# Optimization experiments

Hardware: AMD Instinct MI355X
Metric: run time of the kernel (lower is better)

The kernel has to match this reference:

```python
import jax, jax.numpy as jnp
import numpy as np

B = 64            # batch
C = 23            # chromosomes
E = 1024          # embedding_dim (eos)
D = 1024          # d_model
BOT = 128         # bottleneck_dim (embedding table width)
BINS = 8192       # bins per chromosome (num_bins_list entries)
NUM_BINS = C * BINS
S = 3             # num_states


def setup_inputs() -> dict:
    key = jax.random.key(0)
    ks = jax.random.split(key, 7)
    eos_emb = jax.random.normal(ks[0], (B, C, E), dtype=jnp.float32)
    # embedding table: indices used are 1..NUM_BINS (cum starts at 1), so NUM_BINS+2 rows
    emb_table = jax.random.normal(ks[1], (NUM_BINS + 2, BOT), dtype=jnp.float32) * 0.02
    Wb = jax.random.normal(ks[2], (D, BOT), dtype=jnp.float32) * 0.02   # bin_projection (no bias)
    We = jax.random.normal(ks[3], (D, E), dtype=jnp.float32) * 0.02     # eos_projection weight
    be = jax.random.normal(ks[4], (D,), dtype=jnp.float32) * 0.02       # eos_projection bias
    Wfc = jax.random.normal(ks[5], (S, 2 * D), dtype=jnp.float32) * 0.02  # fc weight
    bfc = jax.random.normal(ks[6], (S,), dtype=jnp.float32) * 0.02        # fc bias
    return {"eos_emb": eos_emb, "emb_table": emb_table, "Wb": Wb,
            "We": We, "be": be, "Wfc": Wfc, "bfc": bfc}


def reference(eos_emb, emb_table, Wb, We, be, Wfc, bfc):
    # eos_projection (use_eos_proj=True): [B, C, E] -> [B, C, D]
    eos = jnp.einsum('bce,de->bcd', eos_emb, We) + be
    # embedding lookup for all bins: indices 1..NUM_BINS (contiguous across chromosomes)
    idx = 1 + jnp.arange(NUM_BINS)
    # bin_projection (bottleneck_dim != d_model): [NUM_BINS, BOT] -> [NUM_BINS, D]
    bin_emb = jnp.einsum('nk,dk->nd', emb_table[idx], Wb).reshape(C, BINS, D)
    # fc on concat([bin_emb, eos]) == bin_emb @ W1^T + eos @ W2^T + b (avoids materializing concat)
    W1, W2 = Wfc[:, :D], Wfc[:, D:]
    part_bin = jnp.einsum('cnd,sd->cns', bin_emb, W1)   # [C, BINS, S]
    part_eos = jnp.einsum('bcd,sd->bcs', eos, W2)        # [B, C, S]
    # original returns list of 23 tensors [B, BINS, S]; stacked here as [B, C, BINS, S]
    out = jax.nn.relu(part_bin[None] + part_eos[:, :, None, :] + bfc)
    return out
```

## Files before the change

### kernel.cpp

```cpp
#include <hip/hip_runtime.h>

#define B_    64
#define C_    23
#define E_    1024
#define D_    1024
#define BOT_  128
#define BINS_ 8192
#define S_    3
#define NUMBINS (C_*BINS_)

typedef float f32x4 __attribute__((ext_vector_type(4)));

#define WS_M  0
#define WS_N  512
#define WS_C0 3584
#define WS_PE 3600

__global__ __launch_bounds__(256) void kprep(const float* __restrict__ Wb,
                                             const float* __restrict__ We,
                                             const float* __restrict__ be,
                                             const float* __restrict__ Wfc,
                                             const float* __restrict__ bfc,
                                             float* __restrict__ ws) {
    const int bx = blockIdx.x;
    const int t  = threadIdx.x;

    if (bx == 72) {
        int wave = t >> 6, lane = t & 63;
        if (wave < 3) {
            const float* w2 = Wfc + wave * 2 * D_ + D_;
            float acc = 0.f;
            #pragma unroll
            for (int j = 0; j < D_ / 64; j++) {
                int d = lane + j * 64;
                acc += w2[d] * be[d];
            }
            #pragma unroll
            for (int off = 32; off; off >>= 1) acc += __shfl_down(acc, off);
            if (lane == 0) ws[WS_C0 + wave] = acc + bfc[wave];
        }
        return;
    }

    __shared__ float wv[3072];
    __shared__ float red[256];

    const int og   = t & 15;
    const int dgrp = t >> 4;

    const float* src;
    int ostride, obase, wofs;
    float* dst0;
    int dstride;

    if (bx < 64) {
        int e0 = bx * 16;
        src = We; ostride = E_; obase = e0; wofs = D_;
        dst0 = ws + WS_N + e0; dstride = E_;
    } else {
        int k0 = (bx - 64) * 16;
        src = Wb; ostride = BOT_; obase = k0; wofs = 0;
        dst0 = ws + WS_M + k0; dstride = BOT_;
    }

    for (int i = t; i < 3072; i += 256) {
        int s = i >> 10, d = i & 1023;
        wv[i] = Wfc[s * 2 * D_ + wofs + d];
    }
    __syncthreads();

    const float* p  = src + (size_t)(dgrp * 64) * ostride + obase + og;
    const float* w0 = wv + dgrp * 64;
    float a0 = 0.f, a1 = 0.f, a2 = 0.f;
    #pragma unroll 8
    for (int i = 0; i < 64; i++) {
        float v = p[(size_t)i * ostride];
        a0 += w0[i] * v;
        a1 += w0[1024 + i] * v;
        a2 += w0[2048 + i] * v;
    }
    float accs[3] = {a0, a1, a2};
    for (int s = 0; s < 3; s++) {
        __syncthreads();
        red[t] = accs[s];
        #pragma unroll
        for (int off = 128; off >= 16; off >>= 1) {
            __syncthreads();
            if (t < off) red[t] += red[t + off];
        }
        if (t < 16) dst0[s * dstride + t] = red[t];
    }
}

__global__ __launch_bounds__(256) void kpe(const float* __restrict__ eos,
                                           float* ws) {
    int wave = threadIdx.x >> 6;
    int lane = threadIdx.x & 63;
    int row  = blockIdx.x * 4 + wave;
    const float* x  = eos + (size_t)row * E_;
    const float* N0 = ws + WS_N;
    float a0 = 0.f, a1 = 0.f, a2 = 0.f;
    #pragma unroll
    for (int j = 0; j < E_ / 64; j++) {
        int i = lane + j * 64;
        float v = x[i];
        a0 += v * N0[i];
        a1 += v * N0[1024 + i];
        a2 += v * N0[2048 + i];
    }
    #pragma unroll
    for (int off = 32; off; off >>= 1) {
        a0 += __shfl_down(a0, off);
        a1 += __shfl_down(a1, off);
        a2 += __shfl_down(a2, off);
    }
    if (lane == 0) {
        float* pe = ws + WS_PE + row * 3;
        pe[0] = a0 + ws[WS_C0 + 0];
        pe[1] = a1 + ws[WS_C0 + 1];
        pe[2] = a2 + ws[WS_C0 + 2];
    }
}

__global__ __launch_bounds__(256) void kmain(const float* __restrict__ table,
                                             const float* __restrict__ ws,
                                             float* __restrict__ out) {
    const int t  = threadIdx.x;
    const int c  = blockIdx.y;
    const int n0 = blockIdx.x * 256;

    const int w  = t >> 6;
    const int l  = t & 63;
    const int h  = l >> 5;
    const int kk = l & 31;

    __shared__ float P[64 * 97];
    __shared__ float pbl[768];
    __shared__ float pel[192];

    f32x4 M0 = ((const f32x4*)(ws + WS_M      ))[kk];
    f32x4 M1 = ((const f32x4*)(ws + WS_M + 128))[kk];
    f32x4 M2 = ((const f32x4*)(ws + WS_M + 256))[kk];

    if (t < 192) {
        int b = t / 3, s = t - b * 3;
        pel[t] = ws[WS_PE + (b * C_ + c) * 3 + s];
    }

    const float* base = table + (size_t)(1 + c * BINS_ + n0) * BOT_ + kk * 4;

    f32x4 va[8], vb[8];
    #pragma unroll
    for (int i = 0; i < 8; i++) {
        int rl = (w * 8 + i) * 2 + h;
        va[i] = *(const f32x4*)(base + (size_t)rl * BOT_);
    }

    #pragma unroll
    for (int bb = 0; bb < 4; bb++) {
        #pragma unroll
        for (int i = 0; i < 8; i++) {
            int rl = (w * 8 + i) * 2 + h;
            f32x4 v = (bb & 1) ? vb[i] : va[i];
            float* pp = &P[rl * 97 + kk * 3];
            pp[0] = v.x * M0.x + v.y * M0.y + v.z * M0.z + v.w * M0.w;
            pp[1] = v.x * M1.x + v.y * M1.y + v.z * M1.z + v.w * M1.w;
            pp[2] = v.x * M2.x + v.y * M2.y + v.z * M2.z + v.w * M2.w;
        }
        if (bb < 3) {
            #pragma unroll
            for (int i = 0; i < 8; i++) {
                int rl = (w * 8 + i) * 2 + h;
                f32x4 ld = *(const f32x4*)(base + (size_t)((bb + 1) * 64 + rl) * BOT_);
                if (bb & 1) va[i] = ld; else vb[i] = ld;
            }
        }
        __syncthreads();
        if (t < 192) {
            int s = t >> 6, ro = t & 63;
            const float* pr = &P[ro * 97 + s];
            float acc = 0.f;
            #pragma unroll
            for (int k = 0; k < 32; k++) acc += pr[k * 3];
            pbl[(bb * 64 + ro) * 3 + s] = acc;
        }
        __syncthreads();
    }

    if (t < 192) {
        f32x4 pv = *(const f32x4*)&pbl[t * 4];
        int s0 = t % 3;
        int s1 = (s0 + 1 == 3) ? 0 : s0 + 1;
        int s2 = (s1 + 1 == 3) ? 0 : s1 + 1;
        for (int b = 0; b < B_; b++) {
            const float* pe = &pel[b * 3];
            f32x4 o;
            o.x = fmaxf(pv.x + pe[s0], 0.f);
            o.y = fmaxf(pv.y + pe[s1], 0.f);
            o.z = fmaxf(pv.z + pe[s2], 0.f);
            o.w = fmaxf(pv.w + pe[s0], 0.f);
            f32x4* dst = (f32x4*)(out + ((size_t)(b * C_ + c) * BINS_ + n0) * 3) + t;
            __builtin_nontemporal_store(o, dst);
        }
    }
}

extern "C" void kernel_launch(void* const* d_in, const int* in_sizes, int n_in,
                              void* d_out, int out_size, void* d_ws, size_t ws_size,
                              hipStream_t stream) {
    const float* eos   = (const float*)d_in[0];
    const float* table = (const float*)d_in[1];
    const float* Wb    = (const float*)d_in[2];
    const float* We    = (const float*)d_in[3];
    const float* be    = (const float*)d_in[4];
    const float* Wfc   = (const float*)d_in[5];
    const float* bfc   = (const float*)d_in[6];
    float* out = (float*)d_out;
    float* ws  = (float*)d_ws;

    kprep<<<73, 256, 0, stream>>>(Wb, We, be, Wfc, bfc, ws);
    kpe<<<368, 256, 0, stream>>>(eos, ws);
    dim3 g(32, 23);
    kmain<<<g, 256, 0, stream>>>(table, ws, out);
}
```

Before: 53.44 us.

## Fuse eos projection into main kernel with global atomic counter barrier

Removes the separate kpe launch. Each of the 736 main blocks now computes two eos rows in two of its waves, publishes them with a release atomic increment, and later spin-waits on the counter until all 1472 rows are done before loading the per-batch offsets. The aim is to drop one kernel launch and its serialization gap, and to overlap the eos dot products with the table loads. The cost is a grid-wide spin barrier, which deadlocks unless all 736 blocks can be resident at once, plus polling overhead.

```diff
diff --git a/kernel.cpp b/kernel.cpp
--- a/kernel.cpp
+++ b/kernel.cpp
@@ -11,10 +11,11 @@
 
 typedef float f32x4 __attribute__((ext_vector_type(4)));
 
-#define WS_M  0
-#define WS_N  512
-#define WS_C0 3584
-#define WS_PE 3600
+#define WS_M   0
+#define WS_N   512
+#define WS_C0  3584
+#define WS_CNT 3590
+#define WS_PE  3600
 
 __global__ __launch_bounds__(256) void kprep(const float* __restrict__ Wb,
                                              const float* __restrict__ We,
@@ -26,6 +27,7 @@
     const int t  = threadIdx.x;
 
     if (bx == 72) {
+        if (t == 0) *(volatile unsigned*)(ws + WS_CNT) = 0u;
         int wave = t >> 6, lane = t & 63;
         if (wave < 3) {
             const float* w2 = Wfc + wave * 2 * D_ + D_;
@@ -92,42 +94,14 @@
     }
 }
 
-__global__ __launch_bounds__(256) void kpe(const float* __restrict__ eos,
-                                           float* ws) {
-    int wave = threadIdx.x >> 6;
-    int lane = threadIdx.x & 63;
-    int row  = blockIdx.x * 4 + wave;
-    const float* x  = eos + (size_t)row * E_;
-    const float* N0 = ws + WS_N;
-    float a0 = 0.f, a1 = 0.f, a2 = 0.f;
-    #pragma unroll
-    for (int j = 0; j < E_ / 64; j++) {
-        int i = lane + j * 64;
-        float v = x[i];
-        a0 += v * N0[i];
-        a1 += v * N0[1024 + i];
-        a2 += v * N0[2048 + i];
-    }
-    #pragma unroll
-    for (int off = 32; off; off >>= 1) {
-        a0 += __shfl_down(a0, off);
-        a1 += __shfl_down(a1, off);
-        a2 += __shfl_down(a2, off);
-    }
-    if (lane == 0) {
-        float* pe = ws + WS_PE + row * 3;
-        pe[0] = a0 + ws[WS_C0 + 0];
-        pe[1] = a1 + ws[WS_C0 + 1];
-        pe[2] = a2 + ws[WS_C0 + 2];
-    }
-}
-
-__global__ __launch_bounds__(256) void kmain(const float* __restrict__ table,
-                                             const float* __restrict__ ws,
-                                             float* __restrict__ out) {
-    const int t  = threadIdx.x;
-    const int c  = blockIdx.y;
-    const int n0 = blockIdx.x * 256;
+__global__ __launch_bounds__(256) void kmainf(const float* __restrict__ table,
+                                              const float* __restrict__ eos,
+                                              float* __restrict__ ws,
+                                              float* __restrict__ out) {
+    const int t   = threadIdx.x;
+    const int bid = blockIdx.x;
+    const int c   = bid >> 5;
+    const int n0  = (bid & 31) * 256;
 
     const int w  = t >> 6;
     const int l  = t & 63;
@@ -138,14 +112,11 @@
     __shared__ float pbl[768];
     __shared__ float pel[192];
 
+    unsigned* cnt = (unsigned*)(ws + WS_CNT);
+
     f32x4 M0 = ((const f32x4*)(ws + WS_M      ))[kk];
     f32x4 M1 = ((const f32x4*)(ws + WS_M + 128))[kk];
     f32x4 M2 = ((const f32x4*)(ws + WS_M + 256))[kk];
-
-    if (t < 192) {
-        int b = t / 3, s = t - b * 3;
-        pel[t] = ws[WS_PE + (b * C_ + c) * 3 + s];
-    }
 
     const float* base = table + (size_t)(1 + c * BINS_ + n0) * BOT_ + kk * 4;
 
@@ -154,6 +125,35 @@
     for (int i = 0; i < 8; i++) {
         int rl = (w * 8 + i) * 2 + h;
         va[i] = *(const f32x4*)(base + (size_t)rl * BOT_);
+    }
+
+    if (w < 2) {
+        int row = 2 * bid + w;
+        const f32x4* x  = (const f32x4*)(eos + (size_t)row * E_);
+        const f32x4* Nq = (const f32x4*)(ws + WS_N);
+        float a0 = 0.f, a1 = 0.f, a2 = 0.f;
+        #pragma unroll
+        for (int j = 0; j < 4; j++) {
+            int q = l + 64 * j;
+            f32x4 v  = x[q];
+            f32x4 q0 = Nq[q], q1 = Nq[256 + q], q2 = Nq[512 + q];
+            a0 += v.x * q0.x + v.y * q0.y + v.z * q0.z + v.w * q0.w;
+            a1 += v.x * q1.x + v.y * q1.y + v.z * q1.z + v.w * q1.w;
+            a2 += v.x * q2.x + v.y * q2.y + v.z * q2.z + v.w * q2.w;
+        }
+        #pragma unroll
+        for (int mask = 32; mask; mask >>= 1) {
+            a0 += __shfl_xor(a0, mask);
+            a1 += __shfl_xor(a1, mask);
+            a2 += __shfl_xor(a2, mask);
+        }
+        if (l == 0) {
+            float* pe = ws + WS_PE + row * 3;
+            pe[0] = a0 + ws[WS_C0 + 0];
+            pe[1] = a1 + ws[WS_C0 + 1];
+            pe[2] = a2 + ws[WS_C0 + 2];
+            __hip_atomic_fetch_add(cnt, 1u, __ATOMIC_RELEASE, __HIP_MEMORY_SCOPE_AGENT);
+        }
     }
 
     #pragma unroll
@@ -186,6 +186,15 @@
         }
         __syncthreads();
     }
+
+    while (__hip_atomic_load(cnt, __ATOMIC_ACQUIRE, __HIP_MEMORY_SCOPE_AGENT) < 1472u)
+        __builtin_amdgcn_s_sleep(2);
+
+    if (t < 192) {
+        int b = t / 3, s = t - b * 3;
+        pel[t] = ws[WS_PE + (b * C_ + c) * 3 + s];
+    }
+    __syncthreads();
 
     if (t < 192) {
         f32x4 pv = *(const f32x4*)&pbl[t * 4];
@@ -219,7 +228,5 @@
     float* ws  = (float*)d_ws;
 
     kprep<<<73, 256, 0, stream>>>(Wb, We, be, Wfc, bfc, ws);
-    kpe<<<368, 256, 0, stream>>>(eos, ws);
-    dim3 g(32, 23);
-    kmain<<<g, 256, 0, stream>>>(table, ws, out);
+    kmainf<<<736, 256, 0, stream>>>(table, eos, ws, out);
 }
```

New measurement: 145.1 us. 171% more time.
